# Kernel tuning notes

Measured on AMD Instinct MI355X. Metric: run time of the kernel, lower is better.

## Reference

```python
import jax, jax.numpy as jnp
import numpy as np

N_HEADS = 16


def setup_inputs() -> dict:
    key = jax.random.key(0)
    ks = jax.random.split(key, 12)
    B, S, D = 2, 2048, 1024
    inp = {
        "query": jax.random.normal(ks[0], (B, S, D), jnp.float32),
        "key": jax.random.normal(ks[1], (B, S, D), jnp.float32),
        "value": jax.random.normal(ks[2], (B, S, D), jnp.float32),
        "mask": jnp.ones((B, S), jnp.int32),
        "Wq": jax.random.normal(ks[3], (D, D), jnp.float32) * 0.02,
        "bq": jax.random.normal(ks[4], (D,), jnp.float32) * 0.02,
        "Wk": jax.random.normal(ks[5], (D, D), jnp.float32) * 0.02,
        "bk": jax.random.normal(ks[6], (D,), jnp.float32) * 0.02,
        "Wv": jax.random.normal(ks[7], (D, D), jnp.float32) * 0.02,
        "bv": jax.random.normal(ks[8], (D,), jnp.float32) * 0.02,
        "Wo": jax.random.normal(ks[9], (D, D), jnp.float32) * 0.02,
        "bo": jax.random.normal(ks[10], (D,), jnp.float32) * 0.02,
    }
    return inp


def _shape(x, bs, n_heads, d_head):
    # (bs, seq, dim) -> (bs, n_heads, seq, d_head)
    return x.reshape(bs, -1, n_heads, d_head).transpose(0, 2, 1, 3)


def reference(query, key, value, mask, Wq, bq, Wk, bk, Wv, bv, Wo, bo):
    bs, q_len, dim = query.shape
    d_head = dim // N_HEADS

    q = _shape(query @ Wq + bq, bs, N_HEADS, d_head) / jnp.sqrt(jnp.asarray(d_head, query.dtype))
    k = _shape(key @ Wk + bk, bs, N_HEADS, d_head)
    v = _shape(value @ Wv + bv, bs, N_HEADS, d_head)

    scores = jnp.einsum("bhqd,bhkd->bhqk", q, k)  # [bs, h, q_len, k_len]
    neg = jnp.finfo(scores.dtype).min
    scores = jnp.where((mask == 0)[:, None, None, :], neg, scores)
    weights = jax.nn.softmax(scores, axis=-1)  # dropout p=0 -> identity

    context = jnp.einsum("bhqk,bhkd->bhqd", weights, v)
    context = context.transpose(0, 2, 1, 3).reshape(bs, q_len, dim)
    return context @ Wo + bo
```

## Files before the change

### kernel.cpp

```cpp
#include <hip/hip_runtime.h>
#include <hip/hip_bf16.h>
#include <stdint.h>

typedef short s16x8 __attribute__((ext_vector_type(8)));
typedef float f32x4 __attribute__((ext_vector_type(4)));
typedef float f32x16 __attribute__((ext_vector_type(16)));

union FragU { uint4 u; s16x8 v; };

static __device__ __forceinline__ uint32_t pk2bf(float a, float b) {
  union { __hip_bfloat162 h; uint32_t u; } cv;
  cv.h = __float22bfloat162_rn(make_float2(a, b));
  return cv.u;
}

static __device__ __forceinline__ unsigned short f2bf(float f) {
  union { float f; uint32_t u; } x; x.f = f;
  uint32_t r = x.u + 0x7FFFu + ((x.u >> 16) & 1u);
  return (unsigned short)(r >> 16);
}

static __device__ __forceinline__ void gl_lds16(const void* g, void* lds_wave_base) {
  __builtin_amdgcn_global_load_lds(
      (const __attribute__((address_space(1))) uint32_t*)(uintptr_t)g,
      (__attribute__((address_space(3))) uint32_t*)(uintptr_t)lds_wave_base, 16, 0, 0);
}

__global__ __launch_bounds__(256) void prep_kernel(const float* __restrict__ W0,
                                                   const float* __restrict__ W1,
                                                   const float* __restrict__ W2,
                                                   const float* __restrict__ W3,
                                                   unsigned short* __restrict__ T0,
                                                   unsigned short* __restrict__ T1,
                                                   unsigned short* __restrict__ T2,
                                                   unsigned short* __restrict__ T3,
                                                   const float* __restrict__ qs,
                                                   const float* __restrict__ ks,
                                                   const float* __restrict__ vs,
                                                   unsigned short* __restrict__ Qc,
                                                   unsigned short* __restrict__ Kc,
                                                   unsigned short* __restrict__ Vc) {
  __shared__ unsigned short tile[64][68];
  const int blk = blockIdx.x;
  const int t = threadIdx.x;
  if (blk < 1024) {
    const int z = blk >> 8;
    const float* W = (z == 0) ? W0 : (z == 1) ? W1 : (z == 2) ? W2 : W3;
    unsigned short* WT = (z == 0) ? T0 : (z == 1) ? T1 : (z == 2) ? T2 : T3;
    const int n0 = (blk & 15) * 64, k0 = ((blk >> 4) & 15) * 64;
    const int r = t >> 4, c4 = (t & 15) * 4;
#pragma unroll
    for (int i = 0; i < 4; ++i) {
      const int k = i * 16 + r;
      const float4 v = *(const float4*)&W[(k0 + k) * 1024 + n0 + c4];
      tile[k][c4 + 0] = f2bf(v.x);
      tile[k][c4 + 1] = f2bf(v.y);
      tile[k][c4 + 2] = f2bf(v.z);
      tile[k][c4 + 3] = f2bf(v.w);
    }
    __syncthreads();
#pragma unroll
    for (int i = 0; i < 4; ++i) {
      const int n = i * 16 + r;
      ushort4 o;
      o.x = tile[c4 + 0][n];
      o.y = tile[c4 + 1][n];
      o.z = tile[c4 + 2][n];
      o.w = tile[c4 + 3][n];
      *(ushort4*)&WT[(n0 + n) * 1024 + k0 + c4] = o;
    }
  } else {
    const int c = blk - 1024;
    const int z = c >> 11, sub = c & 2047;
    const float* src = (z == 0) ? qs : (z == 1) ? ks : vs;
    unsigned short* dst = (z == 0) ? Qc : (z == 1) ? Kc : Vc;
    const size_t base = ((size_t)sub * 256 + t) * 8;
    const float4 f0 = *(const float4*)(src + base);
    const float4 f1 = *(const float4*)(src + base + 4);
    const uint4 o{pk2bf(f0.x, f0.y), pk2bf(f0.z, f0.w), pk2bf(f1.x, f1.y), pk2bf(f1.z, f1.w)};
    *(uint4*)(dst + base) = o;
  }
}

__global__ __launch_bounds__(256) void wt4_kernel(const float* __restrict__ W0,
                                                  const float* __restrict__ W1,
                                                  const float* __restrict__ W2,
                                                  const float* __restrict__ W3,
                                                  unsigned short* __restrict__ T0,
                                                  unsigned short* __restrict__ T1,
                                                  unsigned short* __restrict__ T2,
                                                  unsigned short* __restrict__ T3) {
  __shared__ unsigned short tile[64][68];
  const int z = blockIdx.z;
  const float* W = (z == 0) ? W0 : (z == 1) ? W1 : (z == 2) ? W2 : W3;
  unsigned short* WT = (z == 0) ? T0 : (z == 1) ? T1 : (z == 2) ? T2 : T3;
  const int t = threadIdx.x;
  const int n0 = blockIdx.x * 64, k0 = blockIdx.y * 64;
  const int r = t >> 4, c4 = (t & 15) * 4;
#pragma unroll
  for (int i = 0; i < 4; ++i) {
    const int k = i * 16 + r;
    const float4 v = *(const float4*)&W[(k0 + k) * 1024 + n0 + c4];
    tile[k][c4 + 0] = f2bf(v.x);
    tile[k][c4 + 1] = f2bf(v.y);
    tile[k][c4 + 2] = f2bf(v.z);
    tile[k][c4 + 3] = f2bf(v.w);
  }
  __syncthreads();
#pragma unroll
  for (int i = 0; i < 4; ++i) {
    const int n = i * 16 + r;
    ushort4 o;
    o.x = tile[c4 + 0][n];
    o.y = tile[c4 + 1][n];
    o.z = tile[c4 + 2][n];
    o.w = tile[c4 + 3][n];
    *(ushort4*)&WT[(n0 + n) * 1024 + k0 + c4] = o;
  }
}

__global__ __launch_bounds__(256, 3) void qkv_gemm_bf16(const unsigned short* __restrict__ Aq,
                                                        const unsigned short* __restrict__ Ak,
                                                        const unsigned short* __restrict__ Av,
                                                        const unsigned short* __restrict__ Wq,
                                                        const unsigned short* __restrict__ Wk,
                                                        const unsigned short* __restrict__ Wv,
                                                        const float* __restrict__ bq,
                                                        const float* __restrict__ bk,
                                                        const float* __restrict__ bv,
                                                        unsigned short* __restrict__ Qb,
                                                        unsigned short* __restrict__ Kb,
                                                        unsigned short* __restrict__ Vt,
                                                        const float qscale) {
  __shared__ char AsB[3][8192];
  __shared__ char BsB[3][8192];
  const int t = threadIdx.x;
  const int z = blockIdx.z;
  const unsigned short* A = (z == 0) ? Aq : (z == 1) ? Ak : Av;
  const unsigned short* BT = (z == 0) ? Wq : (z == 1) ? Wk : Wv;
  const float* bias = (z == 0) ? bq : (z == 1) ? bk : bv;
  const float scale = (z == 0) ? qscale : 1.0f;

  const int lane = t & 63, w = t >> 6;
  const int g = lane >> 4, li = lane & 15;
  const int wr = (w >> 1) * 64, wc = (w & 1) * 64;
  const int lin = blockIdx.x + 8 * blockIdx.y;
  const int work = (lin & 7) * 32 + (lin >> 3);
  const int m0 = (work >> 3) * 128, n0 = (work & 7) * 128;

  const int r1 = t >> 2, c1 = (t & 3) ^ ((r1 >> 1) & 3);
  const int r2 = r1 + 64, c2 = (t & 3) ^ ((r2 >> 1) & 3);

  auto stage = [&](int kt, int buf) {
    const int k0 = kt * 32;
    gl_lds16(A + (size_t)(m0 + r1) * 1024 + k0 + c1 * 8, &AsB[buf][0] + (w << 10));
    gl_lds16(A + (size_t)(m0 + r2) * 1024 + k0 + c2 * 8, &AsB[buf][0] + 4096 + (w << 10));
    gl_lds16(BT + (size_t)(n0 + r1) * 1024 + k0 + c1 * 8, &BsB[buf][0] + (w << 10));
    gl_lds16(BT + (size_t)(n0 + r2) * 1024 + k0 + c2 * 8, &BsB[buf][0] + 4096 + (w << 10));
  };

  f32x4 acc[4][4] = {};
  stage(0, 0);
  stage(1, 1);
  asm volatile("s_waitcnt vmcnt(4)" ::: "memory");
  asm volatile("s_barrier" ::: "memory");

  int cur = 0;
  for (int kt = 0; kt < 32; ++kt) {
    if (kt < 30) {
      int nb = cur + 2; if (nb >= 3) nb -= 3;
      stage(kt + 2, nb);
    }
    const char* Ab = &AsB[cur][0];
    const char* Bb = &BsB[cur][0];
    FragU a[4], bf[4];
#pragma unroll
    for (int i = 0; i < 4; ++i) {
      const int ra = wr + i * 16 + li;
      a[i].u = *(const uint4*)(Ab + ra * 64 + ((g ^ ((ra >> 1) & 3)) << 4));
      const int rb = wc + i * 16 + li;
      bf[i].u = *(const uint4*)(Bb + rb * 64 + ((g ^ ((rb >> 1) & 3)) << 4));
    }
#pragma unroll
    for (int fm = 0; fm < 4; ++fm)
#pragma unroll
      for (int fn = 0; fn < 4; ++fn)
        acc[fm][fn] = __builtin_amdgcn_mfma_f32_16x16x32_bf16(a[fm].v, bf[fn].v, acc[fm][fn], 0, 0, 0);

    if (kt < 30) {
      asm volatile("s_waitcnt vmcnt(4)" ::: "memory");
    } else if (kt == 30) {
      asm volatile("s_waitcnt vmcnt(0)" ::: "memory");
    }
    if (kt < 31) asm volatile("s_barrier" ::: "memory");
    cur = (cur == 2) ? 0 : cur + 1;
  }

  unsigned short* OutN = (z == 0) ? Qb : Kb;
#pragma unroll
  for (int fn = 0; fn < 4; ++fn) {
    const int n = n0 + wc + fn * 16 + li;
    const float bv2 = bias[n];
#pragma unroll
    for (int fm = 0; fm < 4; ++fm) {
      const int mb = m0 + wr + fm * 16 + g * 4;
      const f32x4 v = acc[fm][fn];
      ushort4 pk;
      pk.x = f2bf((v[0] + bv2) * scale);
      pk.y = f2bf((v[1] + bv2) * scale);
      pk.z = f2bf((v[2] + bv2) * scale);
      pk.w = f2bf((v[3] + bv2) * scale);
      if (z == 2) {
        const int bb = mb >> 11, s = mb & 2047;
        *(ushort4*)&Vt[(size_t)(bb * 1024 + n) * 2048 + s] = pk;
      } else {
        unsigned short* o = OutN;
        o[(size_t)(mb + 0) * 1024 + n] = pk.x;
        o[(size_t)(mb + 1) * 1024 + n] = pk.y;
        o[(size_t)(mb + 2) * 1024 + n] = pk.z;
        o[(size_t)(mb + 3) * 1024 + n] = pk.w;
      }
    }
  }
}

__global__ __launch_bounds__(256, 3) void qkv_gemm_f32(const float* __restrict__ Aq,
                                                       const float* __restrict__ Ak,
                                                       const float* __restrict__ Av,
                                                       const unsigned short* __restrict__ Wq,
                                                       const unsigned short* __restrict__ Wk,
                                                       const unsigned short* __restrict__ Wv,
                                                       const float* __restrict__ bq,
                                                       const float* __restrict__ bk,
                                                       const float* __restrict__ bv,
                                                       unsigned short* __restrict__ Qb,
                                                       unsigned short* __restrict__ Kb,
                                                       unsigned short* __restrict__ Vt,
                                                       const float qscale) {
  __shared__ unsigned short As[2][128 * 32];
  __shared__ unsigned short Bs[2][128 * 32];
  const int t = threadIdx.x;
  const int z = blockIdx.z;
  const float* A = (z == 0) ? Aq : (z == 1) ? Ak : Av;
  const unsigned short* BT = (z == 0) ? Wq : (z == 1) ? Wk : Wv;
  const float* bias = (z == 0) ? bq : (z == 1) ? bk : bv;
  const float scale = (z == 0) ? qscale : 1.0f;

  const int lane = t & 63, w = t >> 6;
  const int g = lane >> 4, li = lane & 15;
  const int wr = (w >> 1) * 64, wc = (w & 1) * 64;
  const int lin = blockIdx.x + 8 * blockIdx.y;
  const int work = (lin & 7) * 32 + (lin >> 3);
  const int m0 = (work >> 3) * 128, n0 = (work & 7) * 128;

  const int arow = t >> 1, ac0 = (t & 1) * 2, asw = (arow >> 1) & 3;
  const int br1 = t >> 2, bg1 = (t & 3) ^ ((br1 >> 1) & 3);
  const int br2 = br1 + 64, bg2 = (t & 3) ^ ((br2 >> 1) & 3);

  auto stageB = [&](int k0, int buf) {
    gl_lds16(BT + (size_t)(n0 + br1) * 1024 + k0 + bg1 * 8, (char*)&Bs[buf][0] + (w << 10));
    gl_lds16(BT + (size_t)(n0 + br2) * 1024 + k0 + bg2 * 8, (char*)&Bs[buf][0] + 4096 + (w << 10));
  };

  uint4 ar0, ar1;
  auto loadA = [&](int k0) {
    const float* ga = A + (size_t)(m0 + arow) * 1024 + k0 + ac0 * 8;
    const float4 f0 = *(const float4*)(ga + 0), f1 = *(const float4*)(ga + 4);
    const float4 f2 = *(const float4*)(ga + 8), f3 = *(const float4*)(ga + 12);
    ar0 = uint4{pk2bf(f0.x, f0.y), pk2bf(f0.z, f0.w), pk2bf(f1.x, f1.y), pk2bf(f1.z, f1.w)};
    ar1 = uint4{pk2bf(f2.x, f2.y), pk2bf(f2.z, f2.w), pk2bf(f3.x, f3.y), pk2bf(f3.z, f3.w)};
  };
  auto storeA = [&](int buf) {
    char* ab = (char*)&As[buf][0] + arow * 64;
    *(uint4*)(ab + ((ac0 ^ asw) << 4)) = ar0;
    *(uint4*)(ab + (((ac0 + 1) ^ asw) << 4)) = ar1;
  };

  f32x4 acc[4][4] = {};
  stageB(0, 0);
  loadA(0);
  storeA(0);
  __syncthreads();
  int cur = 0;
  for (int k0 = 0; k0 < 1024; k0 += 32) {
    const bool more = (k0 + 32) < 1024;
    if (more) {
      stageB(k0 + 32, cur ^ 1);
      loadA(k0 + 32);
    }
    const char* Ab = (const char*)&As[cur][0];
    const char* Bb = (const char*)&Bs[cur][0];
    FragU a[4], bf[4];
#pragma unroll
    for (int i = 0; i < 4; ++i) {
      const int rowa = wr + i * 16 + li;
      a[i].u = *(const uint4*)(Ab + rowa * 64 + (((g) ^ ((rowa >> 1) & 3)) << 4));
      const int rowb = wc + i * 16 + li;
      bf[i].u = *(const uint4*)(Bb + rowb * 64 + (((g) ^ ((rowb >> 1) & 3)) << 4));
    }
#pragma unroll
    for (int fm = 0; fm < 4; ++fm)
#pragma unroll
      for (int fn = 0; fn < 4; ++fn)
        acc[fm][fn] = __builtin_amdgcn_mfma_f32_16x16x32_bf16(a[fm].v, bf[fn].v, acc[fm][fn], 0, 0, 0);
    if (more) storeA(cur ^ 1);
    __syncthreads();
    cur ^= 1;
  }

  unsigned short* OutN = (z == 0) ? Qb : Kb;
#pragma unroll
  for (int fn = 0; fn < 4; ++fn) {
    const int n = n0 + wc + fn * 16 + li;
    const float bv2 = bias[n];
#pragma unroll
    for (int fm = 0; fm < 4; ++fm) {
      const int mb = m0 + wr + fm * 16 + g * 4;
      const f32x4 v = acc[fm][fn];
      ushort4 pk;
      pk.x = f2bf((v[0] + bv2) * scale);
      pk.y = f2bf((v[1] + bv2) * scale);
      pk.z = f2bf((v[2] + bv2) * scale);
      pk.w = f2bf((v[3] + bv2) * scale);
      if (z == 2) {
        const int bb = mb >> 11, s = mb & 2047;
        *(ushort4*)&Vt[(size_t)(bb * 1024 + n) * 2048 + s] = pk;
      } else {
        unsigned short* o = OutN;
        o[(size_t)(mb + 0) * 1024 + n] = pk.x;
        o[(size_t)(mb + 1) * 1024 + n] = pk.y;
        o[(size_t)(mb + 2) * 1024 + n] = pk.z;
        o[(size_t)(mb + 3) * 1024 + n] = pk.w;
      }
    }
  }
}

__global__ __launch_bounds__(256, 3) void out_gemm(const unsigned short* __restrict__ A,
                                                   const unsigned short* __restrict__ BT,
                                                   const float* __restrict__ bias,
                                                   float* __restrict__ Out) {
  __shared__ char AsB[3][8192];
  __shared__ char BsB[3][8192];
  const int t = threadIdx.x;
  const int lane = t & 63, w = t >> 6;
  const int g = lane >> 4, li = lane & 15;
  const int wr = (w >> 1) * 64, wc = (w & 1) * 64;
  const int lin = blockIdx.x + 8 * blockIdx.y;
  const int work = (lin & 7) * 32 + (lin >> 3);
  const int m0 = (work >> 3) * 128, n0 = (work & 7) * 128;

  const int r1 = t >> 2, c1 = (t & 3) ^ ((r1 >> 1) & 3);
  const int r2 = r1 + 64, c2 = (t & 3) ^ ((r2 >> 1) & 3);

  auto stage = [&](int kt, int buf) {
    const int k0 = kt * 32;
    gl_lds16(A + (size_t)(m0 + r1) * 1024 + k0 + c1 * 8, &AsB[buf][0] + (w << 10));
    gl_lds16(A + (size_t)(m0 + r2) * 1024 + k0 + c2 * 8, &AsB[buf][0] + 4096 + (w << 10));
    gl_lds16(BT + (size_t)(n0 + r1) * 1024 + k0 + c1 * 8, &BsB[buf][0] + (w << 10));
    gl_lds16(BT + (size_t)(n0 + r2) * 1024 + k0 + c2 * 8, &BsB[buf][0] + 4096 + (w << 10));
  };

  f32x4 acc[4][4] = {};
  stage(0, 0);
  stage(1, 1);
  asm volatile("s_waitcnt vmcnt(4)" ::: "memory");
  asm volatile("s_barrier" ::: "memory");

  int cur = 0;
  for (int kt = 0; kt < 32; ++kt) {
    if (kt < 30) {
      int nb = cur + 2; if (nb >= 3) nb -= 3;
      stage(kt + 2, nb);
    }
    const char* Ab = &AsB[cur][0];
    const char* Bb = &BsB[cur][0];
    FragU a[4], bf[4];
#pragma unroll
    for (int i = 0; i < 4; ++i) {
      const int ra = wr + i * 16 + li;
      a[i].u = *(const uint4*)(Ab + ra * 64 + ((g ^ ((ra >> 1) & 3)) << 4));
      const int rb = wc + i * 16 + li;
      bf[i].u = *(const uint4*)(Bb + rb * 64 + ((g ^ ((rb >> 1) & 3)) << 4));
    }
#pragma unroll
    for (int fm = 0; fm < 4; ++fm)
#pragma unroll
      for (int fn = 0; fn < 4; ++fn)
        acc[fm][fn] = __builtin_amdgcn_mfma_f32_16x16x32_bf16(a[fm].v, bf[fn].v, acc[fm][fn], 0, 0, 0);

    if (kt < 30) {
      asm volatile("s_waitcnt vmcnt(4)" ::: "memory");
    } else if (kt == 30) {
      asm volatile("s_waitcnt vmcnt(0)" ::: "memory");
    }
    if (kt < 31) asm volatile("s_barrier" ::: "memory");
    cur = (cur == 2) ? 0 : cur + 1;
  }

#pragma unroll
  for (int fn = 0; fn < 4; ++fn) {
    const int n = n0 + wc + fn * 16 + li;
    const float bv = bias[n];
#pragma unroll
    for (int fm = 0; fm < 4; ++fm) {
      const int mb = m0 + wr + fm * 16 + g * 4;
      const f32x4 v = acc[fm][fn];
#pragma unroll
      for (int r = 0; r < 4; ++r) Out[(size_t)(mb + r) * 1024 + n] = v[r] + bv;
    }
  }
}

__global__ __launch_bounds__(256, 2) void attn_kernel(const unsigned short* __restrict__ Qb,
                                                      const unsigned short* __restrict__ Kb,
                                                      const unsigned short* __restrict__ Vt,
                                                      const int* __restrict__ mask,
                                                      unsigned short* __restrict__ ctx) {
  __shared__ char smem[2][16384];
  const int t = threadIdx.x, lane = t & 63, w = t >> 6;
  const int l31 = lane & 31, hi = lane >> 5;
  const int d0 = blockIdx.x + 16 * blockIdx.y;
  const int work = (d0 & 7) * 64 + (d0 >> 3);
  const int qblk = work & 15, bh = work >> 4;
  const int b = bh >> 4, h = bh & 15;
  const int q0 = qblk * 128;
  const int qrow = b * 2048 + q0 + w * 32 + l31;

  const unsigned short* Kbase = Kb + (size_t)(b * 2048) * 1024 + h * 64;
  const unsigned short* Vbase = Vt + (size_t)(b * 1024 + h * 64) * 2048;

  const int srw = lane >> 3;
  const int ssc = (lane & 7) ^ srw;

  int mv_next;
  auto stage = [&](int i, int buf) {
    const int kv0 = i * 64;
#pragma unroll
    for (int j = 0; j < 2; ++j) {
      const int rr = w * 16 + j * 8 + srw;
      char* ldsb = &smem[buf][0] + w * 2048 + j * 1024;
      gl_lds16(Kbase + (size_t)(kv0 + rr) * 1024 + ssc * 8, ldsb);
      gl_lds16(Vbase + (size_t)rr * 2048 + kv0 + ssc * 8, ldsb + 8192);
    }
    mv_next = mask[b * 2048 + kv0 + lane];
  };

  FragU qf[4];
  {
    const unsigned short* qb = Qb + (size_t)qrow * 1024 + h * 64 + hi * 8;
#pragma unroll
    for (int dc = 0; dc < 4; ++dc) qf[dc].u = *(const uint4*)(qb + dc * 16);
  }

  stage(0, 0);
  asm volatile("s_waitcnt vmcnt(0)" ::: "memory");
  int mv_cur = mv_next;
  asm volatile("s_barrier" ::: "memory");
  __builtin_amdgcn_sched_barrier(0);

  f32x16 acc[2] = {};
  float m_run = 8.0f, l_run = 0.f;
  int cur = 0;

  for (int i = 0; i < 32; ++i) {
    if (i < 31) stage(i + 1, cur ^ 1);
    const int mvcur = mv_cur;
    const char* Ksp = &smem[cur][0];
    const char* Vsp = &smem[cur][8192];

    f32x16 sc[2] = {};
    {
      __builtin_amdgcn_s_setprio(1);
#pragma unroll
      for (int t2 = 0; t2 < 2; ++t2) {
        const int row = t2 * 32 + l31;
        const int sw = (row & 7) << 4;
        const int rb = row * 128;
#pragma unroll
        for (int dc = 0; dc < 4; ++dc) {
          FragU kf;
          kf.u = *(const uint4*)(Ksp + rb + ((16 * (dc * 2 + hi)) ^ sw));
          sc[t2] = __builtin_amdgcn_mfma_f32_32x32x16_bf16(kf.v, qf[dc].v, sc[t2], 0, 0, 0);
        }
      }
      __builtin_amdgcn_s_setprio(0);
    }

    if (!__all(mvcur != 0)) {
#pragma unroll
      for (int t2 = 0; t2 < 2; ++t2)
#pragma unroll
        for (int r = 0; r < 16; ++r) {
          const int kvv = t2 * 32 + (r & 3) + 8 * (r >> 2) + 4 * hi;
          sc[t2][r] += (__shfl(mvcur, kvv, 64) ? 0.f : -30000.f);
        }
    }

    float pm = sc[0][0];
#pragma unroll
    for (int t2 = 0; t2 < 2; ++t2)
#pragma unroll
      for (int r = 0; r < 16; ++r) pm = fmaxf(pm, sc[t2][r]);
    pm = fmaxf(pm, __shfl_xor(pm, 32, 64));

    if (!__all(pm <= m_run + 8.f)) {
      const float m_new = fmaxf(m_run, pm);
      const float rsc = __builtin_amdgcn_exp2f(m_run - m_new);
      m_run = m_new;
      l_run *= rsc;
#pragma unroll
      for (int dt = 0; dt < 2; ++dt)
#pragma unroll
        for (int r = 0; r < 16; ++r) acc[dt][r] *= rsc;
    }

    float rs = 0.f;
#pragma unroll
    for (int t2 = 0; t2 < 2; ++t2)
#pragma unroll
      for (int r = 0; r < 16; ++r) {
        const float e = __builtin_amdgcn_exp2f(sc[t2][r] - m_run);
        sc[t2][r] = e;
        rs += e;
      }
    l_run += rs;

    FragU pf[4];
#pragma unroll
    for (int ks = 0; ks < 4; ++ks) {
      const int t2 = ks >> 1, s8 = (ks & 1) * 8;
      uint32_t U = pk2bf(sc[t2][s8 + 0], sc[t2][s8 + 1]);
      uint32_t V2 = pk2bf(sc[t2][s8 + 2], sc[t2][s8 + 3]);
      uint32_t X = pk2bf(sc[t2][s8 + 4], sc[t2][s8 + 5]);
      uint32_t Y = pk2bf(sc[t2][s8 + 6], sc[t2][s8 + 7]);
      asm("v_permlane32_swap_b32 %0, %1" : "+v"(U), "+v"(X));
      asm("v_permlane32_swap_b32 %0, %1" : "+v"(V2), "+v"(Y));
      pf[ks].u = uint4{U, V2, X, Y};
    }

    {
      __builtin_amdgcn_s_setprio(1);
#pragma unroll
      for (int dt = 0; dt < 2; ++dt) {
        const int drow = dt * 32 + l31;
        const int sw = (drow & 7) << 4;
        const int rb = drow * 128;
#pragma unroll
        for (int ks = 0; ks < 4; ++ks) {
          FragU vf;
          vf.u = *(const uint4*)(Vsp + rb + ((16 * (ks * 2 + hi)) ^ sw));
          acc[dt] = __builtin_amdgcn_mfma_f32_32x32x16_bf16(vf.v, pf[ks].v, acc[dt], 0, 0, 0);
        }
      }
      __builtin_amdgcn_s_setprio(0);
    }

    if (i < 31) {
      asm volatile("s_waitcnt vmcnt(0)" ::: "memory");
      mv_cur = mv_next;
      asm volatile("s_barrier" ::: "memory");
      __builtin_amdgcn_sched_barrier(0);
      cur ^= 1;
    }
  }

  const float l_tot = l_run + __shfl_xor(l_run, 32, 64);
  const float inv_l = 1.0f / l_tot;
  unsigned short* cb = ctx + (size_t)qrow * 1024 + h * 64;
#pragma unroll
  for (int dt = 0; dt < 2; ++dt)
#pragma unroll
    for (int rq = 0; rq < 4; ++rq) {
      uint2 o;
      o.x = pk2bf(acc[dt][rq * 4 + 0] * inv_l, acc[dt][rq * 4 + 1] * inv_l);
      o.y = pk2bf(acc[dt][rq * 4 + 2] * inv_l, acc[dt][rq * 4 + 3] * inv_l);
      *(uint2*)(cb + dt * 32 + rq * 8 + hi * 4) = o;
    }
}

extern "C" void kernel_launch(void* const* d_in, const int* in_sizes, int n_in,
                              void* d_out, int out_size, void* d_ws, size_t ws_size,
                              hipStream_t stream) {
  const float* query = (const float*)d_in[0];
  const float* key = (const float*)d_in[1];
  const float* value = (const float*)d_in[2];
  const int* mask = (const int*)d_in[3];
  const float* Wq = (const float*)d_in[4];
  const float* bq = (const float*)d_in[5];
  const float* Wk = (const float*)d_in[6];
  const float* bk = (const float*)d_in[7];
  const float* Wv = (const float*)d_in[8];
  const float* bv = (const float*)d_in[9];
  const float* Wo = (const float*)d_in[10];
  const float* bo = (const float*)d_in[11];
  float* out = (float*)d_out;

  const size_t MB = 1024 * 1024;
  if (ws_size < 40 * MB) return;
  char* ws = (char*)d_ws;
  unsigned short* WqT = (unsigned short*)(ws);
  unsigned short* WkT = (unsigned short*)(ws + 2 * MB);
  unsigned short* WvT = (unsigned short*)(ws + 4 * MB);
  unsigned short* WoT = (unsigned short*)(ws + 6 * MB);
  unsigned short* Qb = (unsigned short*)(ws + 8 * MB);
  unsigned short* Kb = (unsigned short*)(ws + 16 * MB);
  unsigned short* Vt = (unsigned short*)(ws + 24 * MB);
  unsigned short* ctx = (unsigned short*)(ws + 32 * MB);

  const dim3 tb(256);
  const float qscale = 0.125f * 1.4426950408889634f;

  if (ws_size >= 64 * MB) {
    unsigned short* Qc = (unsigned short*)(ws + 40 * MB);
    unsigned short* Kc = (unsigned short*)(ws + 48 * MB);
    unsigned short* Vc = (unsigned short*)(ws + 56 * MB);
    prep_kernel<<<dim3(7168), tb, 0, stream>>>(Wq, Wk, Wv, Wo, WqT, WkT, WvT, WoT,
                                               query, key, value, Qc, Kc, Vc);
    qkv_gemm_bf16<<<dim3(8, 32, 3), tb, 0, stream>>>(Qc, Kc, Vc, WqT, WkT, WvT,
                                                     bq, bk, bv, Qb, Kb, Vt, qscale);
  } else {
    wt4_kernel<<<dim3(16, 16, 4), tb, 0, stream>>>(Wq, Wk, Wv, Wo, WqT, WkT, WvT, WoT);
    qkv_gemm_f32<<<dim3(8, 32, 3), tb, 0, stream>>>(query, key, value, WqT, WkT, WvT,
                                                    bq, bk, bv, Qb, Kb, Vt, qscale);
  }

  attn_kernel<<<dim3(16, 32), tb, 0, stream>>>(Qb, Kb, Vt, mask, ctx);

  out_gemm<<<dim3(8, 32), tb, 0, stream>>>(ctx, WoT, bo, out);
}
```

Measured before the change: 125.1 us.

## Software-pipeline attention with triple-buffered register-staged KV and narrower out-GEMM tiles

The attention kernel now loads K/V tiles into registers and stores them to LDS itself, replacing direct global-to-LDS loads. It triple-buffers the tiles and overlaps the QK^T MFMAs of the next tile with the softmax and PV of the current one, keeping two score sets alive. This is meant to hide softmax latency behind matrix work, at the cost of more registers and LDS per block. Separately, the output GEMM tile shrinks from 128x128 to 128x64, doubling the grid to improve occupancy and CU coverage, at the price of less operand reuse.

```diff
diff --git a/kernel.cpp b/kernel.cpp
--- a/kernel.cpp
+++ b/kernel.cpp
@@ -341,14 +341,14 @@
                                                    const float* __restrict__ bias,
                                                    float* __restrict__ Out) {
   __shared__ char AsB[3][8192];
-  __shared__ char BsB[3][8192];
+  __shared__ char BsB[3][4096];
   const int t = threadIdx.x;
   const int lane = t & 63, w = t >> 6;
   const int g = lane >> 4, li = lane & 15;
-  const int wr = (w >> 1) * 64, wc = (w & 1) * 64;
-  const int lin = blockIdx.x + 8 * blockIdx.y;
-  const int work = (lin & 7) * 32 + (lin >> 3);
-  const int m0 = (work >> 3) * 128, n0 = (work & 7) * 128;
+  const int wr = (w >> 1) * 64, wc = (w & 1) * 32;
+  const int lin = blockIdx.x + 16 * blockIdx.y;
+  const int work = (lin & 7) * 64 + (lin >> 3);
+  const int m0 = (work >> 4) * 128, n0 = (work & 15) * 64;
 
   const int r1 = t >> 2, c1 = (t & 3) ^ ((r1 >> 1) & 3);
   const int r2 = r1 + 64, c2 = (t & 3) ^ ((r2 >> 1) & 3);
@@ -358,13 +358,12 @@
     gl_lds16(A + (size_t)(m0 + r1) * 1024 + k0 + c1 * 8, &AsB[buf][0] + (w << 10));
     gl_lds16(A + (size_t)(m0 + r2) * 1024 + k0 + c2 * 8, &AsB[buf][0] + 4096 + (w << 10));
     gl_lds16(BT + (size_t)(n0 + r1) * 1024 + k0 + c1 * 8, &BsB[buf][0] + (w << 10));
-    gl_lds16(BT + (size_t)(n0 + r2) * 1024 + k0 + c2 * 8, &BsB[buf][0] + 4096 + (w << 10));
-  };
-
-  f32x4 acc[4][4] = {};
+  };
+
+  f32x4 acc[4][2] = {};
   stage(0, 0);
   stage(1, 1);
-  asm volatile("s_waitcnt vmcnt(4)" ::: "memory");
+  asm volatile("s_waitcnt vmcnt(3)" ::: "memory");
   asm volatile("s_barrier" ::: "memory");
 
   int cur = 0;
@@ -375,22 +374,25 @@
     }
     const char* Ab = &AsB[cur][0];
     const char* Bb = &BsB[cur][0];
-    FragU a[4], bf[4];
+    FragU a[4], bf[2];
 #pragma unroll
     for (int i = 0; i < 4; ++i) {
       const int ra = wr + i * 16 + li;
       a[i].u = *(const uint4*)(Ab + ra * 64 + ((g ^ ((ra >> 1) & 3)) << 4));
-      const int rb = wc + i * 16 + li;
-      bf[i].u = *(const uint4*)(Bb + rb * 64 + ((g ^ ((rb >> 1) & 3)) << 4));
+    }
+#pragma unroll
+    for (int j = 0; j < 2; ++j) {
+      const int rb = wc + j * 16 + li;
+      bf[j].u = *(const uint4*)(Bb + rb * 64 + ((g ^ ((rb >> 1) & 3)) << 4));
     }
 #pragma unroll
     for (int fm = 0; fm < 4; ++fm)
 #pragma unroll
-      for (int fn = 0; fn < 4; ++fn)
+      for (int fn = 0; fn < 2; ++fn)
         acc[fm][fn] = __builtin_amdgcn_mfma_f32_16x16x32_bf16(a[fm].v, bf[fn].v, acc[fm][fn], 0, 0, 0);
 
     if (kt < 30) {
-      asm volatile("s_waitcnt vmcnt(4)" ::: "memory");
+      asm volatile("s_waitcnt vmcnt(3)" ::: "memory");
     } else if (kt == 30) {
       asm volatile("s_waitcnt vmcnt(0)" ::: "memory");
     }
@@ -399,7 +401,7 @@
   }
 
 #pragma unroll
-  for (int fn = 0; fn < 4; ++fn) {
+  for (int fn = 0; fn < 2; ++fn) {
     const int n = n0 + wc + fn * 16 + li;
     const float bv = bias[n];
 #pragma unroll
@@ -417,7 +419,7 @@
                                                       const unsigned short* __restrict__ Vt,
                                                       const int* __restrict__ mask,
                                                       unsigned short* __restrict__ ctx) {
-  __shared__ char smem[2][16384];
+  __shared__ char smem[3][16384];
   const int t = threadIdx.x, lane = t & 63, w = t >> 6;
   const int l31 = lane & 31, hi = lane >> 5;
   const int d0 = blockIdx.x + 16 * blockIdx.y;
@@ -427,23 +429,29 @@
   const int q0 = qblk * 128;
   const int qrow = b * 2048 + q0 + w * 32 + l31;
 
+  const int srow = t >> 3, sch = t & 7;
+
   const unsigned short* Kbase = Kb + (size_t)(b * 2048) * 1024 + h * 64;
   const unsigned short* Vbase = Vt + (size_t)(b * 1024 + h * 64) * 2048;
-
-  const int srw = lane >> 3;
-  const int ssc = (lane & 7) ^ srw;
-
-  int mv_next;
-  auto stage = [&](int i, int buf) {
-    const int kv0 = i * 64;
-#pragma unroll
-    for (int j = 0; j < 2; ++j) {
-      const int rr = w * 16 + j * 8 + srw;
-      char* ldsb = &smem[buf][0] + w * 2048 + j * 1024;
-      gl_lds16(Kbase + (size_t)(kv0 + rr) * 1024 + ssc * 8, ldsb);
-      gl_lds16(Vbase + (size_t)rr * 2048 + kv0 + ssc * 8, ldsb + 8192);
-    }
-    mv_next = mask[b * 2048 + kv0 + lane];
+  const int* mbase = mask + b * 2048 + lane;
+
+  uint4 kr0, kr1, vr0, vr1;
+  auto loadKV = [&](int i) {
+    const int kvn = i * 64;
+    kr0 = *(const uint4*)(Kbase + (size_t)(kvn + srow) * 1024 + sch * 8);
+    kr1 = *(const uint4*)(Kbase + (size_t)(kvn + srow + 32) * 1024 + sch * 8);
+    vr0 = *(const uint4*)(Vbase + (size_t)srow * 2048 + kvn + sch * 8);
+    vr1 = *(const uint4*)(Vbase + (size_t)(srow + 32) * 2048 + kvn + sch * 8);
+  };
+  auto storeKV = [&](char* bufp) {
+    char* kb = bufp;
+    char* vb = bufp + 8192;
+    const int o0 = srow * 128 + ((sch * 16) ^ ((srow & 7) << 4));
+    const int o1 = (srow + 32) * 128 + ((sch * 16) ^ ((srow & 7) << 4));
+    *(uint4*)(kb + o0) = kr0;
+    *(uint4*)(kb + o1) = kr1;
+    *(uint4*)(vb + o0) = vr0;
+    *(uint4*)(vb + o1) = vr1;
   };
 
   FragU qf[4];
@@ -453,40 +461,29 @@
     for (int dc = 0; dc < 4; ++dc) qf[dc].u = *(const uint4*)(qb + dc * 16);
   }
 
-  stage(0, 0);
-  asm volatile("s_waitcnt vmcnt(0)" ::: "memory");
-  int mv_cur = mv_next;
-  asm volatile("s_barrier" ::: "memory");
-  __builtin_amdgcn_sched_barrier(0);
-
   f32x16 acc[2] = {};
   float m_run = 8.0f, l_run = 0.f;
-  int cur = 0;
-
-  for (int i = 0; i < 32; ++i) {
-    if (i < 31) stage(i + 1, cur ^ 1);
-    const int mvcur = mv_cur;
-    const char* Ksp = &smem[cur][0];
-    const char* Vsp = &smem[cur][8192];
-
-    f32x16 sc[2] = {};
-    {
-      __builtin_amdgcn_s_setprio(1);
-#pragma unroll
-      for (int t2 = 0; t2 < 2; ++t2) {
-        const int row = t2 * 32 + l31;
-        const int sw = (row & 7) << 4;
-        const int rb = row * 128;
-#pragma unroll
-        for (int dc = 0; dc < 4; ++dc) {
-          FragU kf;
-          kf.u = *(const uint4*)(Ksp + rb + ((16 * (dc * 2 + hi)) ^ sw));
-          sc[t2] = __builtin_amdgcn_mfma_f32_32x32x16_bf16(kf.v, qf[dc].v, sc[t2], 0, 0, 0);
-        }
+
+  auto QK = [&](f32x16 (&sc)[2], const char* kb) {
+#pragma unroll
+    for (int r = 0; r < 16; ++r) { sc[0][r] = 0.f; sc[1][r] = 0.f; }
+    __builtin_amdgcn_s_setprio(1);
+#pragma unroll
+    for (int t2 = 0; t2 < 2; ++t2) {
+      const int row = t2 * 32 + l31;
+      const int sw = (row & 7) << 4;
+      const int rb = row * 128;
+#pragma unroll
+      for (int dc = 0; dc < 4; ++dc) {
+        FragU kf;
+        kf.u = *(const uint4*)(kb + rb + ((16 * (dc * 2 + hi)) ^ sw));
+        sc[t2] = __builtin_amdgcn_mfma_f32_32x32x16_bf16(kf.v, qf[dc].v, sc[t2], 0, 0, 0);
       }
-      __builtin_amdgcn_s_setprio(0);
-    }
-
+    }
+    __builtin_amdgcn_s_setprio(0);
+  };
+
+  auto SOFTPV = [&](f32x16 (&sc)[2], int mvcur, const char* vb) {
     if (!__all(mvcur != 0)) {
 #pragma unroll
       for (int t2 = 0; t2 < 2; ++t2)
@@ -539,30 +536,62 @@
       pf[ks].u = uint4{U, V2, X, Y};
     }
 
+    __builtin_amdgcn_s_setprio(1);
+#pragma unroll
+    for (int dt = 0; dt < 2; ++dt) {
+      const int drow = dt * 32 + l31;
+      const int sw = (drow & 7) << 4;
+      const int rb = drow * 128;
+#pragma unroll
+      for (int ks = 0; ks < 4; ++ks) {
+        FragU vf;
+        vf.u = *(const uint4*)(vb + rb + ((16 * (ks * 2 + hi)) ^ sw));
+        acc[dt] = __builtin_amdgcn_mfma_f32_32x32x16_bf16(vf.v, pf[ks].v, acc[dt], 0, 0, 0);
+      }
+    }
+    __builtin_amdgcn_s_setprio(0);
+  };
+
+  loadKV(0); storeKV(&smem[0][0]);
+  loadKV(1); storeKV(&smem[1][0]);
+  loadKV(2);
+  __syncthreads();
+
+  char* bE = &smem[0][0];
+  char* bO = &smem[1][0];
+  char* bN = &smem[2][0];
+
+  f32x16 scA[2], scB[2];
+  QK(scA, bE);
+
+  for (int k = 0; k < 15; ++k) {
     {
-      __builtin_amdgcn_s_setprio(1);
-#pragma unroll
-      for (int dt = 0; dt < 2; ++dt) {
-        const int drow = dt * 32 + l31;
-        const int sw = (drow & 7) << 4;
-        const int rb = drow * 128;
-#pragma unroll
-        for (int ks = 0; ks < 4; ++ks) {
-          FragU vf;
-          vf.u = *(const uint4*)(Vsp + rb + ((16 * (ks * 2 + hi)) ^ sw));
-          acc[dt] = __builtin_amdgcn_mfma_f32_32x32x16_bf16(vf.v, pf[ks].v, acc[dt], 0, 0, 0);
-        }
-      }
-      __builtin_amdgcn_s_setprio(0);
-    }
-
-    if (i < 31) {
-      asm volatile("s_waitcnt vmcnt(0)" ::: "memory");
-      mv_cur = mv_next;
-      asm volatile("s_barrier" ::: "memory");
-      __builtin_amdgcn_sched_barrier(0);
-      cur ^= 1;
-    }
+      const int i = 2 * k;
+      const int mv = mbase[i * 64];
+      QK(scB, bO);
+      storeKV(bN);
+      if (i + 3 < 32) loadKV(i + 3);
+      SOFTPV(scA, mv, bE + 8192);
+      __syncthreads();
+      char* tmp = bE; bE = bO; bO = bN; bN = tmp;
+    }
+    {
+      const int i = 2 * k + 1;
+      const int mv = mbase[i * 64];
+      QK(scA, bO);
+      storeKV(bN);
+      if (i + 3 < 32) loadKV(i + 3);
+      SOFTPV(scB, mv, bE + 8192);
+      __syncthreads();
+      char* tmp = bE; bE = bO; bO = bN; bN = tmp;
+    }
+  }
+  {
+    const int mv30 = mbase[30 * 64];
+    const int mv31 = mbase[31 * 64];
+    QK(scB, bO);
+    SOFTPV(scA, mv30, bE + 8192);
+    SOFTPV(scB, mv31, bO + 8192);
   }
 
   const float l_tot = l_run + __shfl_xor(l_run, 32, 64);
@@ -627,5 +656,5 @@
 
   attn_kernel<<<dim3(16, 32), tb, 0, stream>>>(Qb, Kb, Vt, mask, ctx);
 
-  out_gemm<<<dim3(8, 32), tb, 0, stream>>>(ctx, WoT, bo, out);
-}
+  out_gemm<<<dim3(16, 32), tb, 0, stream>>>(ctx, WoT, bo, out);
+}
```

Result: faster. 122.4 us (-2.1%).
